# Kernel tuning notes

Measured on AMD Instinct MI355X. Metric: run time of the kernel, lower is better.

## Reference

```python
import jax, jax.numpy as jnp
import numpy as np

B, S, D_MODEL = 2, 2048, 2048
N_HEADS, N_KV_HEADS = 32, 8
HEAD_DIM = D_MODEL // N_HEADS  # 64


def setup_inputs() -> dict:
    key = jax.random.key(0)
    ks = jax.random.split(key, 7)
    # rope frequencies (as in standard RoPE; values just need to be the right shape)
    inv_freq = 1.0 / (10000.0 ** (jnp.arange(0, HEAD_DIM, 2, dtype=jnp.float32) / HEAD_DIM))
    t = jnp.arange(S, dtype=jnp.float32)
    freqs = t[:, None] * inv_freq[None, :]  # (S, head_dim//2)
    scale = 0.02
    return {
        "x": jax.random.normal(ks[0], (B, S, D_MODEL), jnp.float32),
        "cos": jnp.cos(freqs),
        "sin": jnp.sin(freqs),
        "Wq": jax.random.normal(ks[1], (N_HEADS * HEAD_DIM, D_MODEL), jnp.float32) * scale,
        "Wk": jax.random.normal(ks[2], (N_KV_HEADS * HEAD_DIM, D_MODEL), jnp.float32) * scale,
        "Wv": jax.random.normal(ks[3], (N_KV_HEADS * HEAD_DIM, D_MODEL), jnp.float32) * scale,
        "Wo": jax.random.normal(ks[4], (D_MODEL, D_MODEL), jnp.float32) * scale,
    }


def _apply_rope(x, cos, sin):
    # x: (B, H, S, D); cos/sin: (S, D//2)
    d = x.shape[-1]
    x1, x2 = x[..., : d // 2], x[..., d // 2:]
    c = cos[None, None]
    s = sin[None, None]
    return jnp.concatenate([x1 * c - x2 * s, x1 * s + x2 * c], axis=-1)


def reference(x, cos, sin, Wq, Wk, Wv, Wo):
    b, s, _ = x.shape
    hd = 2 * cos.shape[-1]
    h = Wq.shape[0] // hd
    kv = Wk.shape[0] // hd
    g = h // kv  # query heads per kv head

    q = (x @ Wq.T).reshape(b, s, h, hd).transpose(0, 2, 1, 3)    # (b,h,s,d)
    k = (x @ Wk.T).reshape(b, s, kv, hd).transpose(0, 2, 1, 3)   # (b,kv,s,d)
    v = (x @ Wv.T).reshape(b, s, kv, hd).transpose(0, 2, 1, 3)

    q = _apply_rope(q, cos, sin)
    k = _apply_rope(k, cos, sin)

    # GQA: group query heads instead of materializing repeated K/V
    qg = q.reshape(b, kv, g, s, hd)
    scale = 1.0 / jnp.sqrt(jnp.asarray(hd, x.dtype))
    scores = jnp.einsum('bkgsd,bktd->bkgst', qg, k) * scale      # (b,kv,g,s,s)
    causal = jnp.arange(s)[:, None] >= jnp.arange(s)[None, :]
    scores = jnp.where(causal[None, None, None], scores, jnp.asarray(-jnp.inf, scores.dtype))
    attn = jax.nn.softmax(scores, axis=-1)
    out = jnp.einsum('bkgst,bktd->bkgsd', attn, v)               # (b,kv,g,s,d)
    out = out.reshape(b, h, s, hd).transpose(0, 2, 1, 3).reshape(b, s, h * hd)
    return out @ Wo.T
```

## Files before the change

kernel.cpp:

```cpp
#include <hip/hip_runtime.h>
#include <hip/hip_bf16.h>

typedef __bf16 bf16;
typedef __attribute__((ext_vector_type(8))) __bf16 bf16x8;
typedef __attribute__((ext_vector_type(4))) __bf16 bf16x4;
typedef __attribute__((ext_vector_type(4))) float f32x4;

#define B_SZ 2
#define S_SZ 2048
#define D_SZ 2048
#define H_SZ 32
#define KV_SZ 8
#define HD_SZ 64
#define M_SZ (B_SZ * S_SZ)
#define NQKV 3072

#define GLDS(g, s) __builtin_amdgcn_global_load_lds( \
    (const __attribute__((address_space(1))) void*)(g), \
    (__attribute__((address_space(3))) void*)(s), 16, 0, 0)

__device__ __forceinline__ void bar_lgkm() {
    asm volatile("s_waitcnt lgkmcnt(0)\n\ts_barrier" ::: "memory");
}

__global__ void cvt_all(const float* __restrict__ x, const float* __restrict__ Wq,
                        const float* __restrict__ Wk, const float* __restrict__ Wv,
                        const float* __restrict__ Wo,
                        bf16* __restrict__ xb, bf16* __restrict__ Wf, bf16* __restrict__ wob,
                        int nx, int n1, int n2) {
    int i = blockIdx.x * blockDim.x + threadIdx.x;
    const float* src; bf16* dst; int off;
    if (i < nx)                 { src = x;  dst = xb; off = i; }
    else {
        int j = i - nx;
        if (j < n1)             { src = Wq; dst = Wf; off = j; }
        else if (j < n1 + n2)   { src = Wk; dst = Wf + (size_t)4 * n1; off = j - n1; }
        else if (j < n1 + 2*n2) { src = Wv; dst = Wf + (size_t)4 * (n1 + n2); off = j - n1 - n2; }
        else if (j < 2*n1+2*n2) { src = Wo; dst = wob; off = j - n1 - 2 * n2; }
        else return;
    }
    float4 v = ((const float4*)src)[off];
    bf16x4 o;
    o.x = (bf16)v.x; o.y = (bf16)v.y; o.z = (bf16)v.z; o.w = (bf16)v.w;
    ((bf16x4*)dst)[off] = o;
}

#define GEMM_CORE5(A_, B_, Kdim)                                                 \
    const int tid  = threadIdx.x;                                                \
    const int wv   = tid >> 6;                                                   \
    const int lane = tid & 63;                                                   \
    const int c = lane & 15, quad = lane >> 4;                                   \
    const int wr = wv >> 1, wc = wv & 1;                                         \
    const int g8 = lane >> 3;                                                    \
    const int chs = ((lane & 7) ^ g8) * 8;                                       \
    const int rowBase = blockIdx.y * 128;                                        \
    const int colBase = blockIdx.x * 128;                                        \
    const bf16* Ag = A_ + (size_t)(rowBase + wv * 32 + g8) * Kdim + chs;         \
    const bf16* Bg = B_ + (size_t)(colBase + wv * 32 + g8) * Kdim + chs;         \
    f32x4 acc[4][4] = {};                                                        \
    _Pragma("unroll")                                                            \
    for (int j = 0; j < 4; j++) {           \
        GLDS(Ag + (size_t)(j * 8) * Kdim, Ls + (wv * 32 + j * 8) * 64);          \
        GLDS(Bg + (size_t)(j * 8) * Kdim, Ls + 8192 + (wv * 32 + j * 8) * 64);   \
    }                                                                            \
    for (int k0 = 0; k0 < Kdim; k0 += 64) {                                      \
        bf16* Asb = Ls + ((k0 >> 6) & 1) * 16384;                                \
        bf16* Bsb = Asb + 8192;                                                  \
        if (k0 + 64 < Kdim) {                \
            bf16* Asn = Ls + ((((k0 >> 6) & 1) ^ 1) * 16384);                    \
            _Pragma("unroll")                                                    \
            for (int j = 0; j < 4; j++) {                                        \
                GLDS(Ag + (size_t)(j * 8) * Kdim + (k0 + 64),                    \
                     Asn + (wv * 32 + j * 8) * 64);                              \
                GLDS(Bg + (size_t)(j * 8) * Kdim + (k0 + 64),                    \
                     Asn + 8192 + (wv * 32 + j * 8) * 64);                       \
            }                                                                    \
            asm volatile("s_waitcnt vmcnt(8)" ::: "memory");                     \
        } else {                                                                 \
            asm volatile("s_waitcnt vmcnt(0)" ::: "memory");                     \
        }                                                                        \
        asm volatile("s_waitcnt lgkmcnt(0)\n\ts_barrier" ::: "memory");          \
        _Pragma("unroll")                                                        \
        for (int ks = 0; ks < 2; ks++) {                                         \
            bf16x8 af[4], bfr[4];                                                \
            _Pragma("unroll")                                                    \
            for (int mi = 0; mi < 4; mi++)                                       \
                af[mi] = *(const bf16x8*)(Asb + (wr * 64 + mi * 16 + c) * 64     \
                                          + (((ks << 2) + quad) ^ (c & 7)) * 8); \
            _Pragma("unroll")                                                    \
            for (int ni = 0; ni < 4; ni++)                                       \
                bfr[ni] = *(const bf16x8*)(Bsb + (wc * 64 + ni * 16 + c) * 64    \
                                          + (((ks << 2) + quad) ^ (c & 7)) * 8); \
            _Pragma("unroll")                                                    \
            for (int mi = 0; mi < 4; mi++)                                       \
                _Pragma("unroll")                                                \
                for (int ni = 0; ni < 4; ni++)                                   \
                    acc[mi][ni] = __builtin_amdgcn_mfma_f32_16x16x32_bf16(       \
                        af[mi], bfr[ni], acc[mi][ni], 0, 0, 0);                  \
        }                                                                        \
        asm volatile("s_waitcnt lgkmcnt(0)\n\ts_barrier" ::: "memory");          \
    }                                                                            \
    const int mBase = rowBase + wr * 64;                                         \
    const int nBase = colBase + wc * 64;

__global__ __launch_bounds__(256, 2)
void gemm_qkv(const bf16* __restrict__ A, const bf16* __restrict__ Bw,
              bf16* __restrict__ Qb, bf16* __restrict__ Kb, bf16* __restrict__ Vtb,
              const float* __restrict__ cosp, const float* __restrict__ sinp,
              float qscale)
{
    __shared__ __align__(16) bf16 Ls[2 * 16384];

    GEMM_CORE5(A, Bw, D_SZ)

    const int hcol = nBase;
    if (hcol < 2560) {
        bf16* dst; int hh, Hn; float sc;
        if (hcol < 2048) { dst = Qb; hh = hcol >> 6;        Hn = H_SZ;  sc = qscale; }
        else             { dst = Kb; hh = (hcol >> 6) - 32; Hn = KV_SZ; sc = 1.0f;  }
#pragma unroll
        for (int mi = 0; mi < 4; mi++) {
#pragma unroll
            for (int r = 0; r < 4; r++) {
                int row = mBase + mi * 16 + quad * 4 + r;
                int b = row >> 11;
                int s = row & 2047;
                const float* cr = cosp + (size_t)s * 32;
                const float* sr = sinp + (size_t)s * 32;
                size_t base = ((size_t)(b * Hn + hh) * S_SZ + s) * 64;
#pragma unroll
                for (int nj = 0; nj < 2; nj++) {
                    int d = nj * 16 + c;
                    float x1 = acc[mi][nj][r];
                    float x2 = acc[mi][nj + 2][r];
                    float cv = cr[d], sv = sr[d];
                    dst[base + d]      = (bf16)((x1 * cv - x2 * sv) * sc);
                    dst[base + d + 32] = (bf16)((x1 * sv + x2 * cv) * sc);
                }
            }
        }
    } else {
        const int kvh = (hcol >> 6) - 40;
        const int b   = mBase >> 11;
        const int s0  = mBase & 2047;
#pragma unroll
        for (int nj = 0; nj < 4; nj++) {
            int d = nj * 16 + c;
            size_t base = ((size_t)(b * KV_SZ + kvh) * 64 + d) * (size_t)S_SZ;
#pragma unroll
            for (int mi = 0; mi < 4; mi++) {
                int s = s0 + mi * 16 + quad * 4;
#pragma unroll
                for (int r = 0; r < 4; r++)
                    Vtb[base + s + r] = (bf16)acc[mi][nj][r];
            }
        }
    }
}

__global__ __launch_bounds__(256, 2)
void gemm_out(const bf16* __restrict__ A, const bf16* __restrict__ Bw,
              float* __restrict__ Co, int N, int K)
{
    __shared__ __align__(16) bf16 Ls[2 * 16384];

    GEMM_CORE5(A, Bw, K)

#pragma unroll
    for (int mi = 0; mi < 4; mi++)
#pragma unroll
        for (int ni = 0; ni < 4; ni++) {
            int col = nBase + ni * 16 + c;
#pragma unroll
            for (int r = 0; r < 4; r++) {
                int row = mBase + mi * 16 + quad * 4 + r;
                Co[(size_t)row * N + col] = acc[mi][ni][r];
            }
        }
}

#define PST 72

__global__ __launch_bounds__(256, 3)
void flash_attn(const bf16* __restrict__ Q, const bf16* __restrict__ Kc,
                const bf16* __restrict__ Vt, bf16* __restrict__ Aout)
{
    __shared__ __align__(16) bf16 Ks[64 * 64];
    __shared__ __align__(16) bf16 Vs[64 * 64];
    __shared__ __align__(16) bf16 Ps[2 * 4 * 16 * PST];

    const int tid  = threadIdx.x;
    const int lane = tid & 63;
    const int wave = tid >> 6;
    const int c = lane & 15, quad = lane >> 4;
    const int qloc = wave * 16 + c;

    const int i  = (blockIdx.x + blockIdx.y) & 15;
    const int tA = 31 - i, tB = i;
    const int q0A = tA << 6, q0B = tB << 6;

    const int bh = blockIdx.y;
    const int b  = bh >> 5;
    const int h  = bh & 31;
    const int kv = h >> 2;

    const bf16* Qp = Q  + (size_t)bh * (S_SZ * 64);
    const bf16* Kp = Kc + (size_t)(b * KV_SZ + kv) * (S_SZ * 64);
    const bf16* Vp = Vt + (size_t)(b * KV_SZ + kv) * (64 * S_SZ);

    bf16x8 aqA[2], aqB[2];
    {
        const bf16* qa = Qp + (size_t)(q0A + qloc) * 64 + quad * 8;
        aqA[0] = *(const bf16x8*)qa;  aqA[1] = *(const bf16x8*)(qa + 32);
        const bf16* qb = Qp + (size_t)(q0B + qloc) * 64 + quad * 8;
        aqB[0] = *(const bf16x8*)qb;  aqB[1] = *(const bf16x8*)(qb + 32);
    }

    f32x4 oA[4] = {}, oB[4] = {};
    f32x4 lA = {}, lB = {};

    bf16x8 ones;
#pragma unroll
    for (int j = 0; j < 8; j++) ones[j] = (bf16)1.0f;

    const int srow = tid >> 3;
    const int ch   = tid & 7;
    const int sws  = (ch ^ (srow & 7)) * 8;
    const bf16* Kg0 = Kp + (size_t)srow * 64 + ch * 8;
    const bf16* Kg1 = Kp + (size_t)(srow + 32) * 64 + ch * 8;
    const bf16* Vg0 = Vp + (size_t)srow * S_SZ + ch * 8;
    const bf16* Vg1 = Vp + (size_t)(srow + 32) * S_SZ + ch * 8;

    uint4 pk0 = *(const uint4*)Kg0, pk1 = *(const uint4*)Kg1;
    uint4 pv0 = *(const uint4*)Vg0, pv1 = *(const uint4*)Vg1;

    bf16* PwA = Ps + wave * 16 * PST;
    bf16* PwB = Ps + (4 + wave) * 16 * PST;

    for (int kt = 0; kt <= tA; kt++) {
        *(uint4*)(Ks + srow * 64 + sws)        = pk0;
        *(uint4*)(Ks + (srow + 32) * 64 + sws) = pk1;
        *(uint4*)(Vs + srow * 64 + sws)        = pv0;
        *(uint4*)(Vs + (srow + 32) * 64 + sws) = pv1;
        if (kt < tA) {
            pk0 = *(const uint4*)(Kg0 + (size_t)(kt + 1) * 4096);
            pk1 = *(const uint4*)(Kg1 + (size_t)(kt + 1) * 4096);
            pv0 = *(const uint4*)(Vg0 + (kt + 1) * 64);
            pv1 = *(const uint4*)(Vg1 + (kt + 1) * 64);
        }
        bar_lgkm();

        const bool doB   = (kt <= tB);
        const bool diagA = (kt == tA);
        const bool diagB = (kt == tB);

        f32x4 scA[4] = {}, scB[4] = {};
#pragma unroll
        for (int ks = 0; ks < 2; ks++) {
            bf16x8 ak4[4];
#pragma unroll
            for (int ni = 0; ni < 4; ni++)
                ak4[ni] = *(const bf16x8*)(Ks + (ni * 16 + c) * 64
                                           + (((ks << 2) + quad) ^ (c & 7)) * 8);
            __builtin_amdgcn_s_setprio(1);
#pragma unroll
            for (int ni = 0; ni < 4; ni++)
                scA[ni] = __builtin_amdgcn_mfma_f32_16x16x32_bf16(ak4[ni], aqA[ks], scA[ni], 0, 0, 0);
            if (doB) {
#pragma unroll
                for (int ni = 0; ni < 4; ni++)
                    scB[ni] = __builtin_amdgcn_mfma_f32_16x16x32_bf16(ak4[ni], aqB[ks], scB[ni], 0, 0, 0);
            }
            __builtin_amdgcn_s_setprio(0);
        }

        if (diagA) {
#pragma unroll
            for (int ni = 0; ni < 4; ni++) {
                bf16x4 pk;
#pragma unroll
                for (int r = 0; r < 4; r++) {
                    float p = exp2f(scA[ni][r]);
                    if ((ni * 16 + quad * 4 + r) > qloc) p = 0.f;
                    pk[r] = (bf16)p;
                }
                *(bf16x4*)(PwA + c * PST + ni * 16 + quad * 4) = pk;
            }
        } else {
#pragma unroll
            for (int ni = 0; ni < 4; ni++) {
                bf16x4 pk;
#pragma unroll
                for (int r = 0; r < 4; r++) pk[r] = (bf16)exp2f(scA[ni][r]);
                *(bf16x4*)(PwA + c * PST + ni * 16 + quad * 4) = pk;
            }
        }
        if (doB) {
            if (diagB) {
#pragma unroll
                for (int ni = 0; ni < 4; ni++) {
                    bf16x4 pk;
#pragma unroll
                    for (int r = 0; r < 4; r++) {
                        float p = exp2f(scB[ni][r]);
                        if ((ni * 16 + quad * 4 + r) > qloc) p = 0.f;
                        pk[r] = (bf16)p;
                    }
                    *(bf16x4*)(PwB + c * PST + ni * 16 + quad * 4) = pk;
                }
            } else {
#pragma unroll
                for (int ni = 0; ni < 4; ni++) {
                    bf16x4 pk;
#pragma unroll
                    for (int r = 0; r < 4; r++) pk[r] = (bf16)exp2f(scB[ni][r]);
                    *(bf16x4*)(PwB + c * PST + ni * 16 + quad * 4) = pk;
                }
            }
        }

#pragma unroll
        for (int ks = 0; ks < 2; ks++) {
            bf16x8 av4[4];
#pragma unroll
            for (int ni = 0; ni < 4; ni++)
                av4[ni] = *(const bf16x8*)(Vs + (ni * 16 + c) * 64
                                           + (((ks << 2) + quad) ^ (c & 7)) * 8);
            bf16x8 bpA = *(const bf16x8*)(PwA + c * PST + ks * 32 + quad * 8);
            __builtin_amdgcn_s_setprio(1);
            lA = __builtin_amdgcn_mfma_f32_16x16x32_bf16(ones, bpA, lA, 0, 0, 0);
#pragma unroll
            for (int ni = 0; ni < 4; ni++)
                oA[ni] = __builtin_amdgcn_mfma_f32_16x16x32_bf16(av4[ni], bpA, oA[ni], 0, 0, 0);
            __builtin_amdgcn_s_setprio(0);
            if (doB) {
                bf16x8 bpB = *(const bf16x8*)(PwB + c * PST + ks * 32 + quad * 8);
                __builtin_amdgcn_s_setprio(1);
                lB = __builtin_amdgcn_mfma_f32_16x16x32_bf16(ones, bpB, lB, 0, 0, 0);
#pragma unroll
                for (int ni = 0; ni < 4; ni++)
                    oB[ni] = __builtin_amdgcn_mfma_f32_16x16x32_bf16(av4[ni], bpB, oB[ni], 0, 0, 0);
                __builtin_amdgcn_s_setprio(0);
            }
        }
        bar_lgkm();
    }

    {
        float ila = 1.f / lA[0];
        float ilb = 1.f / lB[0];
        bf16* pa = Aout + ((size_t)(b * S_SZ + q0A + qloc)) * D_SZ + h * 64;
        bf16* pb = Aout + ((size_t)(b * S_SZ + q0B + qloc)) * D_SZ + h * 64;
#pragma unroll
        for (int ni = 0; ni < 4; ni++) {
            bf16x4 wa, wb;
#pragma unroll
            for (int r = 0; r < 4; r++) {
                wa[r] = (bf16)(oA[ni][r] * ila);
                wb[r] = (bf16)(oB[ni][r] * ilb);
            }
            *(bf16x4*)(pa + ni * 16 + quad * 4) = wa;
            *(bf16x4*)(pb + ni * 16 + quad * 4) = wb;
        }
    }
}

extern "C" void kernel_launch(void* const* d_in, const int* in_sizes, int n_in,
                              void* d_out, int out_size, void* d_ws, size_t ws_size,
                              hipStream_t stream) {
    const float* x    = (const float*)d_in[0];
    const float* cosp = (const float*)d_in[1];
    const float* sinp = (const float*)d_in[2];
    const float* Wq   = (const float*)d_in[3];
    const float* Wk   = (const float*)d_in[4];
    const float* Wv   = (const float*)d_in[5];
    const float* Wo   = (const float*)d_in[6];
    float* out = (float*)d_out;

    const int M = M_SZ;
    const int D = D_SZ;
    const int NKV = KV_SZ * HD_SZ;

    bf16* xb   = (bf16*)d_ws;
    bf16* Wf   = xb  + (size_t)M * D;
    bf16* Qb   = Wf  + (size_t)NQKV * D;
    bf16* Kb   = Qb  + (size_t)M * D;
    bf16* Vtb  = Kb  + (size_t)B_SZ * KV_SZ * S_SZ * 64;
    bf16* wob  = Vtb + (size_t)B_SZ * KV_SZ * 64 * S_SZ;
    bf16* attn = xb;

    const int nx = M * D / 4, n1 = D * D / 4, n2 = NKV * D / 4;

    cvt_all<<<(nx + 2 * n1 + 2 * n2 + 255) / 256, 256, 0, stream>>>(
        x, Wq, Wk, Wv, Wo, xb, Wf, wob, nx, n1, n2);

    const float qscale = 0.125f * 1.44269504089f;

    gemm_qkv<<<dim3(NQKV / 128, M / 128), 256, 0, stream>>>(xb, Wf, Qb, Kb, Vtb, cosp, sinp, qscale);

    flash_attn<<<dim3(16, B_SZ * H_SZ), 256, 0, stream>>>(Qb, Kb, Vtb, attn);

    gemm_out<<<dim3(D / 128, M / 128), 256, 0, stream>>>(attn, wob, out, D, D);
}
```

Before: 276.8 us.

## Restructure flash attention to one query tile per block with 128-key tiles

Replaces the paired-tile scheme, where each block processed a long and a short query tile together, with one 64-row query tile per block over twice as many blocks. Each iteration now loads and processes a 128-key K/V tile. The row sum is accumulated in registers instead of through an extra MFMA against a ones vector. The aim is to halve barrier/loop overhead per key, drop the ones-MFMA, and expose more parallelism. In exchange it gives up the built-in load balancing of the pairing, wastes up to 64 masked keys on the diagonal tile, and raises LDS use per block.

```diff
diff --git a/kernel.cpp b/kernel.cpp
--- a/kernel.cpp
+++ b/kernel.cpp
@@ -179,15 +179,15 @@
         }
 }
 
-#define PST 72
+#define PST 132
 
 __global__ __launch_bounds__(256, 3)
 void flash_attn(const bf16* __restrict__ Q, const bf16* __restrict__ Kc,
                 const bf16* __restrict__ Vt, bf16* __restrict__ Aout)
 {
-    __shared__ __align__(16) bf16 Ks[64 * 64];
-    __shared__ __align__(16) bf16 Vs[64 * 64];
-    __shared__ __align__(16) bf16 Ps[2 * 4 * 16 * PST];
+    __shared__ __align__(16) bf16 Ks[128 * 64];
+    __shared__ __align__(16) bf16 Vs[64 * 128];
+    __shared__ __align__(16) bf16 Ps[4 * 16 * PST];
 
     const int tid  = threadIdx.x;
     const int lane = tid & 63;
@@ -195,9 +195,9 @@
     const int c = lane & 15, quad = lane >> 4;
     const int qloc = wave * 16 + c;
 
-    const int i  = (blockIdx.x + blockIdx.y) & 15;
-    const int tA = 31 - i, tB = i;
-    const int q0A = tA << 6, q0B = tB << 6;
+    const int t  = 31 - ((blockIdx.x + blockIdx.y) & 31);
+    const int q0 = t << 6;
+    const int NP = (t + 2) >> 1;
 
     const int bh = blockIdx.y;
     const int b  = bh >> 5;
@@ -208,159 +208,114 @@
     const bf16* Kp = Kc + (size_t)(b * KV_SZ + kv) * (S_SZ * 64);
     const bf16* Vp = Vt + (size_t)(b * KV_SZ + kv) * (64 * S_SZ);
 
-    bf16x8 aqA[2], aqB[2];
+    bf16x8 aq[2];
     {
-        const bf16* qa = Qp + (size_t)(q0A + qloc) * 64 + quad * 8;
-        aqA[0] = *(const bf16x8*)qa;  aqA[1] = *(const bf16x8*)(qa + 32);
-        const bf16* qb = Qp + (size_t)(q0B + qloc) * 64 + quad * 8;
-        aqB[0] = *(const bf16x8*)qb;  aqB[1] = *(const bf16x8*)(qb + 32);
-    }
-
-    f32x4 oA[4] = {}, oB[4] = {};
-    f32x4 lA = {}, lB = {};
-
-    bf16x8 ones;
-#pragma unroll
-    for (int j = 0; j < 8; j++) ones[j] = (bf16)1.0f;
-
-    const int srow = tid >> 3;
-    const int ch   = tid & 7;
-    const int sws  = (ch ^ (srow & 7)) * 8;
-    const bf16* Kg0 = Kp + (size_t)srow * 64 + ch * 8;
-    const bf16* Kg1 = Kp + (size_t)(srow + 32) * 64 + ch * 8;
-    const bf16* Vg0 = Vp + (size_t)srow * S_SZ + ch * 8;
-    const bf16* Vg1 = Vp + (size_t)(srow + 32) * S_SZ + ch * 8;
-
-    uint4 pk0 = *(const uint4*)Kg0, pk1 = *(const uint4*)Kg1;
-    uint4 pv0 = *(const uint4*)Vg0, pv1 = *(const uint4*)Vg1;
-
-    bf16* PwA = Ps + wave * 16 * PST;
-    bf16* PwB = Ps + (4 + wave) * 16 * PST;
-
-    for (int kt = 0; kt <= tA; kt++) {
-        *(uint4*)(Ks + srow * 64 + sws)        = pk0;
-        *(uint4*)(Ks + (srow + 32) * 64 + sws) = pk1;
-        *(uint4*)(Vs + srow * 64 + sws)        = pv0;
-        *(uint4*)(Vs + (srow + 32) * 64 + sws) = pv1;
-        if (kt < tA) {
-            pk0 = *(const uint4*)(Kg0 + (size_t)(kt + 1) * 4096);
-            pk1 = *(const uint4*)(Kg1 + (size_t)(kt + 1) * 4096);
-            pv0 = *(const uint4*)(Vg0 + (kt + 1) * 64);
-            pv1 = *(const uint4*)(Vg1 + (kt + 1) * 64);
+        const bf16* qa = Qp + (size_t)(q0 + qloc) * 64 + quad * 8;
+        aq[0] = *(const bf16x8*)qa;
+        aq[1] = *(const bf16x8*)(qa + 32);
+    }
+
+    f32x4 o[4] = {};
+    float lsum = 0.f;
+
+    const int sr = tid >> 3;
+    const int ch = tid & 7;
+    const int swk = (ch ^ (sr & 7)) * 8;
+    const int rv = tid >> 2;
+    const int cv = tid & 3;
+
+    const bf16* Kg = Kp + (size_t)sr * 64 + ch * 8;
+    const bf16* Vg = Vp + (size_t)rv * S_SZ + cv * 8;
+
+    uint4 pk[4], pv[4];
+#pragma unroll
+    for (int j = 0; j < 4; j++) {
+        pk[j] = *(const uint4*)(Kg + (size_t)(32 * j) * 64);
+        pv[j] = *(const uint4*)(Vg + j * 32);
+    }
+
+    bf16* Pw = Ps + (wave * 16) * PST;
+
+    for (int kt = 0; kt < NP; kt++) {
+#pragma unroll
+        for (int j = 0; j < 4; j++) {
+            *(uint4*)(Ks + (sr + 32 * j) * 64 + swk) = pk[j];
+            *(uint4*)(Vs + rv * 128 + ((cv + 4 * j) ^ (rv & 7)) * 8) = pv[j];
+        }
+        if (kt + 1 < NP) {
+            const size_t ko = (size_t)(kt + 1) * 128 * 64;
+#pragma unroll
+            for (int j = 0; j < 4; j++) {
+                pk[j] = *(const uint4*)(Kg + ko + (size_t)(32 * j) * 64);
+                pv[j] = *(const uint4*)(Vg + (kt + 1) * 128 + j * 32);
+            }
         }
         bar_lgkm();
 
-        const bool doB   = (kt <= tB);
-        const bool diagA = (kt == tA);
-        const bool diagB = (kt == tB);
-
-        f32x4 scA[4] = {}, scB[4] = {};
-#pragma unroll
-        for (int ks = 0; ks < 2; ks++) {
-            bf16x8 ak4[4];
-#pragma unroll
-            for (int ni = 0; ni < 4; ni++)
-                ak4[ni] = *(const bf16x8*)(Ks + (ni * 16 + c) * 64
-                                           + (((ks << 2) + quad) ^ (c & 7)) * 8);
+        const bool msk = (kt == NP - 1);
+
+#pragma unroll
+        for (int half = 0; half < 2; half++) {
+            f32x4 sc4[4] = {};
+#pragma unroll
+            for (int ks = 0; ks < 2; ks++) {
+                bf16x8 ak4[4];
+#pragma unroll
+                for (int n4 = 0; n4 < 4; n4++)
+                    ak4[n4] = *(const bf16x8*)(Ks + (half * 64 + n4 * 16 + c) * 64
+                                               + (((ks << 2) + quad) ^ (c & 7)) * 8);
+                __builtin_amdgcn_s_setprio(1);
+#pragma unroll
+                for (int n4 = 0; n4 < 4; n4++)
+                    sc4[n4] = __builtin_amdgcn_mfma_f32_16x16x32_bf16(
+                        ak4[n4], aq[ks], sc4[n4], 0, 0, 0);
+                __builtin_amdgcn_s_setprio(0);
+            }
+            const int kbase = kt * 128 + half * 64;
+#pragma unroll
+            for (int n4 = 0; n4 < 4; n4++) {
+                bf16x4 pkk;
+#pragma unroll
+                for (int r = 0; r < 4; r++) {
+                    float p = exp2f(sc4[n4][r]);
+                    if (msk && (kbase + n4 * 16 + quad * 4 + r) > (q0 + qloc)) p = 0.f;
+                    lsum += p;
+                    pkk[r] = (bf16)p;
+                }
+                *(bf16x4*)(Pw + c * PST + half * 64 + n4 * 16 + quad * 4) = pkk;
+            }
+        }
+
+#pragma unroll
+        for (int ks4 = 0; ks4 < 4; ks4++) {
+            bf16x8 av4[4];
+#pragma unroll
+            for (int d4 = 0; d4 < 4; d4++)
+                av4[d4] = *(const bf16x8*)(Vs + (d4 * 16 + c) * 128
+                                           + (((ks4 << 2) + quad) ^ (c & 7)) * 8);
+            bf16x8 bp = *(const bf16x8*)(Pw + c * PST + ks4 * 32 + quad * 8);
             __builtin_amdgcn_s_setprio(1);
 #pragma unroll
-            for (int ni = 0; ni < 4; ni++)
-                scA[ni] = __builtin_amdgcn_mfma_f32_16x16x32_bf16(ak4[ni], aqA[ks], scA[ni], 0, 0, 0);
-            if (doB) {
-#pragma unroll
-                for (int ni = 0; ni < 4; ni++)
-                    scB[ni] = __builtin_amdgcn_mfma_f32_16x16x32_bf16(ak4[ni], aqB[ks], scB[ni], 0, 0, 0);
-            }
+            for (int d4 = 0; d4 < 4; d4++)
+                o[d4] = __builtin_amdgcn_mfma_f32_16x16x32_bf16(
+                    av4[d4], bp, o[d4], 0, 0, 0);
             __builtin_amdgcn_s_setprio(0);
         }
-
-        if (diagA) {
-#pragma unroll
-            for (int ni = 0; ni < 4; ni++) {
-                bf16x4 pk;
-#pragma unroll
-                for (int r = 0; r < 4; r++) {
-                    float p = exp2f(scA[ni][r]);
-                    if ((ni * 16 + quad * 4 + r) > qloc) p = 0.f;
-                    pk[r] = (bf16)p;
-                }
-                *(bf16x4*)(PwA + c * PST + ni * 16 + quad * 4) = pk;
-            }
-        } else {
-#pragma unroll
-            for (int ni = 0; ni < 4; ni++) {
-                bf16x4 pk;
-#pragma unroll
-                for (int r = 0; r < 4; r++) pk[r] = (bf16)exp2f(scA[ni][r]);
-                *(bf16x4*)(PwA + c * PST + ni * 16 + quad * 4) = pk;
-            }
-        }
-        if (doB) {
-            if (diagB) {
-#pragma unroll
-                for (int ni = 0; ni < 4; ni++) {
-                    bf16x4 pk;
-#pragma unroll
-                    for (int r = 0; r < 4; r++) {
-                        float p = exp2f(scB[ni][r]);
-                        if ((ni * 16 + quad * 4 + r) > qloc) p = 0.f;
-                        pk[r] = (bf16)p;
-                    }
-                    *(bf16x4*)(PwB + c * PST + ni * 16 + quad * 4) = pk;
-                }
-            } else {
-#pragma unroll
-                for (int ni = 0; ni < 4; ni++) {
-                    bf16x4 pk;
-#pragma unroll
-                    for (int r = 0; r < 4; r++) pk[r] = (bf16)exp2f(scB[ni][r]);
-                    *(bf16x4*)(PwB + c * PST + ni * 16 + quad * 4) = pk;
-                }
-            }
-        }
-
-#pragma unroll
-        for (int ks = 0; ks < 2; ks++) {
-            bf16x8 av4[4];
-#pragma unroll
-            for (int ni = 0; ni < 4; ni++)
-                av4[ni] = *(const bf16x8*)(Vs + (ni * 16 + c) * 64
-                                           + (((ks << 2) + quad) ^ (c & 7)) * 8);
-            bf16x8 bpA = *(const bf16x8*)(PwA + c * PST + ks * 32 + quad * 8);
-            __builtin_amdgcn_s_setprio(1);
-            lA = __builtin_amdgcn_mfma_f32_16x16x32_bf16(ones, bpA, lA, 0, 0, 0);
-#pragma unroll
-            for (int ni = 0; ni < 4; ni++)
-                oA[ni] = __builtin_amdgcn_mfma_f32_16x16x32_bf16(av4[ni], bpA, oA[ni], 0, 0, 0);
-            __builtin_amdgcn_s_setprio(0);
-            if (doB) {
-                bf16x8 bpB = *(const bf16x8*)(PwB + c * PST + ks * 32 + quad * 8);
-                __builtin_amdgcn_s_setprio(1);
-                lB = __builtin_amdgcn_mfma_f32_16x16x32_bf16(ones, bpB, lB, 0, 0, 0);
-#pragma unroll
-                for (int ni = 0; ni < 4; ni++)
-                    oB[ni] = __builtin_amdgcn_mfma_f32_16x16x32_bf16(av4[ni], bpB, oB[ni], 0, 0, 0);
-                __builtin_amdgcn_s_setprio(0);
-            }
-        }
         bar_lgkm();
     }
 
     {
-        float ila = 1.f / lA[0];
-        float ilb = 1.f / lB[0];
-        bf16* pa = Aout + ((size_t)(b * S_SZ + q0A + qloc)) * D_SZ + h * 64;
-        bf16* pb = Aout + ((size_t)(b * S_SZ + q0B + qloc)) * D_SZ + h * 64;
-#pragma unroll
-        for (int ni = 0; ni < 4; ni++) {
-            bf16x4 wa, wb;
-#pragma unroll
-            for (int r = 0; r < 4; r++) {
-                wa[r] = (bf16)(oA[ni][r] * ila);
-                wb[r] = (bf16)(oB[ni][r] * ilb);
-            }
-            *(bf16x4*)(pa + ni * 16 + quad * 4) = wa;
-            *(bf16x4*)(pb + ni * 16 + quad * 4) = wb;
+        float s = lsum;
+        s += __shfl_xor(s, 16);
+        s += __shfl_xor(s, 32);
+        float il = 1.f / s;
+        bf16* pa = Aout + ((size_t)(b * S_SZ + q0 + qloc)) * D_SZ + h * 64;
+#pragma unroll
+        for (int d4 = 0; d4 < 4; d4++) {
+            bf16x4 w;
+#pragma unroll
+            for (int r = 0; r < 4; r++) w[r] = (bf16)(o[d4][r] * il);
+            *(bf16x4*)(pa + d4 * 16 + quad * 4) = w;
         }
     }
 }
@@ -398,7 +353,7 @@
 
     gemm_qkv<<<dim3(NQKV / 128, M / 128), 256, 0, stream>>>(xb, Wf, Qb, Kb, Vtb, cosp, sinp, qscale);
 
-    flash_attn<<<dim3(16, B_SZ * H_SZ), 256, 0, stream>>>(Qb, Kb, Vtb, attn);
+    flash_attn<<<dim3(32, B_SZ * H_SZ), 256, 0, stream>>>(Qb, Kb, Vtb, attn);
 
     gemm_out<<<dim3(D / 128, M / 128), 256, 0, stream>>>(attn, wob, out, D, D);
 }
```

Measured after the change: 435.0 us. 57.1% more time.

## Double-buffer K/V tiles in LDS via direct global-to-LDS loads in flash attention

Applied to the files above, without the earlier changes.

Replaces register-staged K/V prefetch and per-iteration stores to shared memory with global_load_lds DMA into a two-slot LDS ring. The next tile loads into the alternate buffer while the current one is consumed, with vmcnt waits controlling readiness. This drops VGPR staging and the LDS store instructions, at the cost of doubled K/V LDS footprint, which may reduce occupancy. The source-side XOR swizzle keeps the same bank-conflict-avoiding layout.

```diff
diff --git a/kernel.cpp b/kernel.cpp
--- a/kernel.cpp
+++ b/kernel.cpp
@@ -185,8 +185,8 @@
 void flash_attn(const bf16* __restrict__ Q, const bf16* __restrict__ Kc,
                 const bf16* __restrict__ Vt, bf16* __restrict__ Aout)
 {
-    __shared__ __align__(16) bf16 Ks[64 * 64];
-    __shared__ __align__(16) bf16 Vs[64 * 64];
+    __shared__ __align__(16) bf16 Ksh[2][64 * 64];
+    __shared__ __align__(16) bf16 Vsh[2][64 * 64];
     __shared__ __align__(16) bf16 Ps[2 * 4 * 16 * PST];
 
     const int tid  = threadIdx.x;
@@ -223,32 +223,39 @@
 #pragma unroll
     for (int j = 0; j < 8; j++) ones[j] = (bf16)1.0f;
 
-    const int srow = tid >> 3;
-    const int ch   = tid & 7;
-    const int sws  = (ch ^ (srow & 7)) * 8;
-    const bf16* Kg0 = Kp + (size_t)srow * 64 + ch * 8;
-    const bf16* Kg1 = Kp + (size_t)(srow + 32) * 64 + ch * 8;
-    const bf16* Vg0 = Vp + (size_t)srow * S_SZ + ch * 8;
-    const bf16* Vg1 = Vp + (size_t)(srow + 32) * S_SZ + ch * 8;
-
-    uint4 pk0 = *(const uint4*)Kg0, pk1 = *(const uint4*)Kg1;
-    uint4 pv0 = *(const uint4*)Vg0, pv1 = *(const uint4*)Vg1;
+    const int g8  = lane >> 3;
+    const int chs = ((lane & 7) ^ g8) * 8;
+    const bf16* KgL = Kp + (size_t)(wave * 16 + g8) * 64 + chs;
+    const bf16* VgL = Vp + (size_t)(wave * 16 + g8) * S_SZ + chs;
 
     bf16* PwA = Ps + wave * 16 * PST;
     bf16* PwB = Ps + (4 + wave) * 16 * PST;
 
+#pragma unroll
+    for (int j = 0; j < 2; j++) {
+        GLDS(KgL + (size_t)(j * 8) * 64,   &Ksh[0][(wave * 16 + j * 8) * 64]);
+        GLDS(VgL + (size_t)(j * 8) * S_SZ, &Vsh[0][(wave * 16 + j * 8) * 64]);
+    }
+
     for (int kt = 0; kt <= tA; kt++) {
-        *(uint4*)(Ks + srow * 64 + sws)        = pk0;
-        *(uint4*)(Ks + (srow + 32) * 64 + sws) = pk1;
-        *(uint4*)(Vs + srow * 64 + sws)        = pv0;
-        *(uint4*)(Vs + (srow + 32) * 64 + sws) = pv1;
+        const int cur = kt & 1;
         if (kt < tA) {
-            pk0 = *(const uint4*)(Kg0 + (size_t)(kt + 1) * 4096);
-            pk1 = *(const uint4*)(Kg1 + (size_t)(kt + 1) * 4096);
-            pv0 = *(const uint4*)(Vg0 + (kt + 1) * 64);
-            pv1 = *(const uint4*)(Vg1 + (kt + 1) * 64);
-        }
-        bar_lgkm();
+            const int nxt = cur ^ 1;
+#pragma unroll
+            for (int j = 0; j < 2; j++) {
+                GLDS(KgL + (size_t)(kt + 1) * 4096 + (size_t)(j * 8) * 64,
+                     &Ksh[nxt][(wave * 16 + j * 8) * 64]);
+                GLDS(VgL + (kt + 1) * 64 + (size_t)(j * 8) * S_SZ,
+                     &Vsh[nxt][(wave * 16 + j * 8) * 64]);
+            }
+            asm volatile("s_waitcnt vmcnt(4)" ::: "memory");
+        } else {
+            asm volatile("s_waitcnt vmcnt(0)" ::: "memory");
+        }
+        asm volatile("s_waitcnt lgkmcnt(0)\n\ts_barrier" ::: "memory");
+
+        const bf16* Kst = Ksh[cur];
+        const bf16* Vst = Vsh[cur];
 
         const bool doB   = (kt <= tB);
         const bool diagA = (kt == tA);
@@ -260,7 +267,7 @@
             bf16x8 ak4[4];
 #pragma unroll
             for (int ni = 0; ni < 4; ni++)
-                ak4[ni] = *(const bf16x8*)(Ks + (ni * 16 + c) * 64
+                ak4[ni] = *(const bf16x8*)(Kst + (ni * 16 + c) * 64
                                            + (((ks << 2) + quad) ^ (c & 7)) * 8);
             __builtin_amdgcn_s_setprio(1);
 #pragma unroll
@@ -324,7 +331,7 @@
             bf16x8 av4[4];
 #pragma unroll
             for (int ni = 0; ni < 4; ni++)
-                av4[ni] = *(const bf16x8*)(Vs + (ni * 16 + c) * 64
+                av4[ni] = *(const bf16x8*)(Vst + (ni * 16 + c) * 64
                                            + (((ks << 2) + quad) ^ (c & 7)) * 8);
             bf16x8 bpA = *(const bf16x8*)(PwA + c * PST + ks * 32 + quad * 8);
             __builtin_amdgcn_s_setprio(1);
```

Result: slower. 293.7 us (+6.1%).
